# Kernel tuning notes

Hardware: AMD Instinct MI355X
Metric: run time of the kernel (lower is better)

Reference implementation:

```python
import jax, jax.numpy as jnp
import numpy as np

HID = 1024
PRED_LEN = 96


def lstm_cell(x, h, c, Wih, Whh, bih, bhh):
    # PyTorch LSTMCell: gates ordered i, f, g, o
    gates = x @ Wih.T + h @ Whh.T + bih + bhh
    i, f, g, o = jnp.split(gates, 4, axis=-1)
    c_new = jax.nn.sigmoid(f) * c + jax.nn.sigmoid(i) * jnp.tanh(g)
    h_new = jax.nn.sigmoid(o) * jnp.tanh(c_new)
    return h_new, c_new


def time_enc(idx, embs):
    # sum of 4 embedding lookups -> [..., time_encode_dim]
    return sum(e[idx[..., k]] for k, e in enumerate(embs))


def setup_inputs() -> dict:
    key = jax.random.key(0)
    ks = jax.random.split(key, 32)
    B, T, IN, OUT, H, TE = 256, 128, 7, 7, HID, 3
    d = {}
    d["x"] = jax.random.normal(ks[0], (B, T, IN), jnp.float32)
    d["y"] = jax.random.normal(ks[1], (B, PRED_LEN, OUT), jnp.float32)
    d["x_time_encode"] = jax.random.randint(ks[2], (B, T, 4), 0, 7)
    d["y_time_encode"] = jax.random.randint(ks[3], (B, PRED_LEN, 4), 0, 7)
    sizes = (12, 31, 24, 7)
    for i, n in enumerate(sizes):
        d[f"emb{i}"] = jax.random.normal(ks[4 + i], (n, TE), jnp.float32)
    ins = (IN + TE, H, H)
    s = float(1.0 / np.sqrt(H))
    for l in range(3):
        d[f"Wih{l}"] = jax.random.uniform(ks[8 + 4 * l], (4 * H, ins[l]), jnp.float32, -s, s)
        d[f"Whh{l}"] = jax.random.uniform(ks[9 + 4 * l], (4 * H, H), jnp.float32, -s, s)
        d[f"bih{l}"] = jax.random.uniform(ks[10 + 4 * l], (4 * H,), jnp.float32, -s, s)
        d[f"bhh{l}"] = jax.random.uniform(ks[11 + 4 * l], (4 * H,), jnp.float32, -s, s)
    d["fcW"] = jax.random.uniform(ks[20], (OUT, H), jnp.float32, -s, s)
    d["fcb"] = jax.random.uniform(ks[21], (OUT,), jnp.float32, -s, s)
    return d


def reference(x, y, x_time_encode, y_time_encode, emb0, emb1, emb2, emb3,
              Wih0, Whh0, bih0, bhh0, Wih1, Whh1, bih1, bhh1,
              Wih2, Whh2, bih2, bhh2, fcW, fcb):
    embs = (emb0, emb1, emb2, emb3)
    layers = ((Wih0, Whh0, bih0, bhh0),
              (Wih1, Whh1, bih1, bhh1),
              (Wih2, Whh2, bih2, bhh2))
    B = x.shape[0]
    H = Whh0.shape[1]

    # encode: concat time embedding, run stacked LSTM over time (dropout_rate=0 -> no-op)
    xin = jnp.concatenate([x, time_enc(x_time_encode, embs)], axis=-1)  # [B,T,in+te]
    h0 = tuple(jnp.zeros((B, H), x.dtype) for _ in range(3))

    def run_layers(hs, cs, inp):
        nh, nc = [], []
        for l, (Wih, Whh, bih, bhh) in enumerate(layers):
            h, c = lstm_cell(inp, hs[l], cs[l], Wih, Whh, bih, bhh)
            nh.append(h)
            nc.append(c)
            inp = h
        return tuple(nh), tuple(nc)

    def enc_step(carry, xt):
        hs, cs = carry
        hs, cs = run_layers(hs, cs, xt)
        return (hs, cs), None

    (hs, cs), _ = jax.lax.scan(enc_step, (h0, h0), xin.swapaxes(0, 1))

    y0 = hs[-1] @ fcW.T + fcb  # [B, out]

    def dec_step(carry, te_idx):
        hs, cs, y_prev = carry
        inp = jnp.concatenate([y_prev, time_enc(te_idx, embs)], axis=-1)
        hs, cs = run_layers(hs, cs, inp)
        yt = hs[-1] @ fcW.T + fcb
        return (hs, cs, yt), yt

    _, ys = jax.lax.scan(dec_step, (hs, cs, y0),
                         y_time_encode[:, :PRED_LEN - 1].swapaxes(0, 1))
    # [B, predict_len, out]
    return jnp.concatenate([y0[:, None], ys.swapaxes(0, 1)], axis=1)
```

## Files before the change

### kernel.cpp

```cpp
#include <hip/hip_runtime.h>

#define HID   1024
#define BATCH 256
#define TSEQ  128
#define PRED  96
#define IND   7
#define OUTD  7
#define SK    10

typedef __attribute__((ext_vector_type(8))) _Float16 f16x8;
typedef __attribute__((ext_vector_type(4))) float    f32x4;

#define BM   64
#define BN   64
#define GSTR 68

#define AUX_COH 17

__device__ __forceinline__ float sigmoidf_fast(float x) {
  return 1.0f / (1.0f + __expf(-x));
}
__device__ __forceinline__ float tanhf_fast(float x) {
  float ax = fabsf(x);
  float e  = __expf(-2.0f * ax);
  float r  = (1.0f - e) / (1.0f + e);
  return copysignf(r, x);
}

template<int AUX>
__device__ __forceinline__ void async_cp16(const void* g, void* l) {
  __builtin_amdgcn_global_load_lds(
      (const __attribute__((address_space(1))) void*)g,
      (__attribute__((address_space(3))) void*)l, 16, 0, AUX);
}

#define WBAR(N) asm volatile("s_waitcnt vmcnt(" #N ")\n\ts_barrier" ::: "memory")
#define BARO()  asm volatile("s_barrier" ::: "memory")

__device__ __forceinline__ void gridbar(unsigned* flags, unsigned* go,
                                        unsigned bc) {
  __syncthreads();
  const int tid = threadIdx.x;
  if (blockIdx.x == 0) {
    if (tid > 0) {
      while (__hip_atomic_load(flags + tid * 32,
                               __ATOMIC_RELAXED, __HIP_MEMORY_SCOPE_SYSTEM) < bc)
        __builtin_amdgcn_s_sleep(1);
    }
    __syncthreads();
    if (tid == 0)
      __hip_atomic_store(go, bc, __ATOMIC_RELAXED, __HIP_MEMORY_SCOPE_SYSTEM);
  } else {
    if (tid == 0) {
      __hip_atomic_store(flags + blockIdx.x * 32, bc,
                         __ATOMIC_RELAXED, __HIP_MEMORY_SCOPE_SYSTEM);
      while (__hip_atomic_load(go, __ATOMIC_RELAXED,
                               __HIP_MEMORY_SCOPE_SYSTEM) < bc)
        __builtin_amdgcn_s_sleep(1);
    }
    __syncthreads();
  }
}

__global__ __launch_bounds__(256) void prep_kernel(
    const float* __restrict__ Wih0, const float* __restrict__ Whh0,
    const float* __restrict__ bih0, const float* __restrict__ bhh0,
    const float* __restrict__ Wih1, const float* __restrict__ Whh1,
    const float* __restrict__ bih1, const float* __restrict__ bhh1,
    const float* __restrict__ Wih2, const float* __restrict__ Whh2,
    const float* __restrict__ bih2, const float* __restrict__ bhh2,
    _Float16* __restrict__ B0, _Float16* __restrict__ B1, _Float16* __restrict__ B2,
    float* __restrict__ W0p, float* __restrict__ biasP)
{
  size_t e = (size_t)blockIdx.x * 256 + threadIdx.x;
  const size_t S0 = (size_t)4096 * 1024;
  const size_t S1 = (size_t)4096 * 2048;
  if (e < S0) {
    int n = (int)(e >> 10), k = (int)(e & 1023);
    int nb = n >> 6, gate = (n >> 4) & 3, u = n & 15;
    int r = gate * 1024 + nb * 16 + u;
    B0[e] = (_Float16)Whh0[(size_t)r * 1024 + k];
  } else if (e < S0 + S1) {
    size_t q = e - S0;
    int n = (int)(q >> 11), k = (int)(q & 2047);
    int nb = n >> 6, gate = (n >> 4) & 3, u = n & 15;
    int r = gate * 1024 + nb * 16 + u;
    float v = (k < 1024) ? Wih1[(size_t)r * 1024 + k]
                         : Whh1[(size_t)r * 1024 + (k - 1024)];
    B1[q] = (_Float16)v;
  } else if (e < S0 + 2 * S1) {
    size_t q = e - S0 - S1;
    int n = (int)(q >> 11), k = (int)(q & 2047);
    int nb = n >> 6, gate = (n >> 4) & 3, u = n & 15;
    int r = gate * 1024 + nb * 16 + u;
    float v = (k < 1024) ? Wih2[(size_t)r * 1024 + k]
// ... 129 lines not shown

#pragma unroll
  for (int i = 0; i < 4; ++i) {
    int m = (tid >> 4) + i * 16;
    int u = tid & 15;
    float gi = Gs[m * GSTR + u];
    float gf = Gs[m * GSTR + 16 + u];
    float gg = Gs[m * GSTR + 32 + u];
    float go = Gs[m * GSTR + 48 + u];
    int nbase = nb * BN;
    gi += bias[nbase + u];
    gf += bias[nbase + 16 + u];
    gg += bias[nbase + 32 + u];
    go += bias[nbase + 48 + u];
    if (layer == 0) {
#pragma unroll
      for (int k = 0; k < SK; ++k) {
        float sv = SmallIn[m * SK + k];
        gi += sv * W0s[u * 11 + k];
        gf += sv * W0s[(16 + u) * 11 + k];
        gg += sv * W0s[(32 + u) * 11 + k];
        go += sv * W0s[(48 + u) * 11 + k];
      }
    }
    size_t cidx = (size_t)(Mbase + m) * HID + (size_t)nb * 16 + u;
    float cold = cst[cidx];
    float cn = sigmoidf_fast(gf) * cold + sigmoidf_fast(gi) * tanhf_fast(gg);
    float hn = sigmoidf_fast(go) * tanhf_fast(cn);
    cst[cidx] = cn;
    ho[cidx] = (_Float16)hn;
  }
}

template<int KC, int MODE>
__device__ __forceinline__ void dec_layer(
    const char* A1, const char* A2, const char* Bm,
    const int* a_off, const int* b_off, const int* l_off,
    char* smem, float* Gs, const float* SmallIn, const float* W0s,
    const float* biasg, float* creg, _Float16* hout, float* out,
    const float* w7, const float* fcadd, int s, int Mbase, int nb, int tid)
{
  const int w = tid >> 6, lane = tid & 63;
  const int quad = lane >> 4, l16 = lane & 15;
  f32x4 acc[4] = {};

#define DISSUE(c) do { \
    const char* Ab_ = (KC == 8 || (c) < 8) ? (A1 + (size_t)(c) * 256) \
                                           : (A2 + (size_t)((c) - 8) * 256); \
    const char* Bb_ = Bm + (size_t)(c) * 256; \
    char* Lb_ = smem + ((c) % 4) * 32768; \
    _Pragma("unroll") \
    for (int i_ = 0; i_ < 4; ++i_) { \
      async_cp16<AUX_COH>(Ab_ + a_off[i_], Lb_ + l_off[i_]); \
      async_cp16<0>(Bb_ + b_off[i_], Lb_ + 16384 + l_off[i_]); \
    } } while (0)

  DISSUE(0);
  DISSUE(1);
  DISSUE(2);
#pragma unroll
  for (int c = 0; c < KC; ++c) {
    if (c + 3 < KC)       { DISSUE(c + 3); WBAR(24); }
    else if (c + 3 == KC) { WBAR(16); }
    else if (c + 2 == KC) { WBAR(8); }
    else                  { WBAR(0); }
    const _Float16* As = (const _Float16*)(smem + (c % 4) * 32768);
    const _Float16* Bs = As + 8192;
#pragma unroll
    for (int ks = 0; ks < 4; ++ks) {
      int sq = (ks * 4 + quad) ^ l16;
      f16x8 bf = *reinterpret_cast<const f16x8*>(Bs + (w * 16 + l16) * 128 + sq * 8);
#pragma unroll
      for (int mt = 0; mt < 4; ++mt) {
        f16x8 af = *reinterpret_cast<const f16x8*>(As + (mt * 16 + l16) * 128 + sq * 8);
        acc[mt] = __builtin_amdgcn_mfma_f32_16x16x32_f16(af, bf, acc[mt], 0, 0, 0);
      }
    }
    BARO();
  }
#undef DISSUE

#pragma unroll
  for (int mt = 0; mt < 4; ++mt) {
    int row = mt * 16 + quad * 4;
    int col = w * 16 + l16;
#pragma unroll
    for (int r = 0; r < 4; ++r)
      Gs[(row + r) * GSTR + col] = acc[mt][r];
  }
  __syncthreads();

#pragma unroll
  for (int i = 0; i < 4; ++i) {
    int m = (tid >> 4) + i * 16;
    int u = tid & 15;
    float gi = Gs[m * GSTR + u]      + biasg[0];
    float gf = Gs[m * GSTR + 16 + u] + biasg[1];
    float gg = Gs[m * GSTR + 32 + u] + biasg[2];
    float go = Gs[m * GSTR + 48 + u] + biasg[3];
    if (MODE == 1) {
#pragma unroll
      for (int k = 0; k < SK; ++k) {
        float sv = SmallIn[m * SK + k];
        gi += sv * W0s[u * 11 + k];
        gf += sv * W0s[(16 + u) * 11 + k];
        gg += sv * W0s[(32 + u) * 11 + k];
        go += sv * W0s[(48 + u) * 11 + k];
      }
    }
    float cn = sigmoidf_fast(gf) * creg[i] + sigmoidf_fast(gi) * tanhf_fast(gg);
    float hn = sigmoidf_fast(go) * tanhf_fast(cn);
    creg[i] = cn;
    union { _Float16 f; unsigned short us; } cv; cv.f = (_Float16)hn;
    __hip_atomic_store(
        (unsigned short*)(hout + (size_t)(Mbase + m) * HID + (size_t)nb * 16 + u),
        cv.us, __ATOMIC_RELAXED, __HIP_MEMORY_SCOPE_SYSTEM);
    if (MODE == 3) {
#pragma unroll
      for (int o = 0; o < OUTD; ++o) {
        float r = hn * w7[o];
        r += __shfl_xor(r, 1, 16);
        r += __shfl_xor(r, 2, 16);
        r += __shfl_xor(r, 4, 16);
        r += __shfl_xor(r, 8, 16);
        if (u == 0)
          atomicAdd(&out[(size_t)(Mbase + m) * (PRED * OUTD) + (s + 1) * OUTD + o],
                    r + fcadd[o]);
      }
    }
  }
}

__global__ __launch_bounds__(256, 1) void lstm_dec(
    _Float16* __restrict__ h0a, _Float16* __restrict__ h0b,
    _Float16* __restrict__ h1a, _Float16* __restrict__ h1b,
    _Float16* __restrict__ h2a, _Float16* __restrict__ h2b,
    const _Float16* __restrict__ B0g, const _Float16* __restrict__ B1g,
    const _Float16* __restrict__ B2g,
    const float* __restrict__ biasP, const float* __restrict__ W0p,
    const float* __restrict__ cbuf,
    float* __restrict__ out, const int* __restrict__ yte,
    const float* __restrict__ e0, const float* __restrict__ e1,
    const float* __restrict__ e2, const float* __restrict__ e3,
    const float* __restrict__ fcW, const float* __restrict__ fcb,
    unsigned* __restrict__ flags, unsigned* __restrict__ go_w)
{
  __shared__ __align__(16) char smem[4 * 32768];
  __shared__ float Gs[BM * GSTR];
  __shared__ float SmallIn[BM * SK];
  __shared__ float W0s[BN * 11];

  const int tid = threadIdx.x;
  const int nb = blockIdx.x & 63, mb = blockIdx.x >> 6;
  const int Mbase = mb * BM;
  const int w = tid >> 6, lane = tid & 63;
  const int dr = lane >> 4, ds = lane & 15;

  int a_off[4], b1_off[4], b2_off[4], l_off[4];
#pragma unroll
  for (int i = 0; i < 4; ++i) {
    int lrow = w * 16 + i * 4 + dr;
    int sg = ds ^ (i * 4 + dr);
    a_off[i]  = (Mbase + lrow) * 2048 + sg * 16;
    b1_off[i] = (nb * 64 + lrow) * 2048 + sg * 16;
    b2_off[i] = (nb * 64 + lrow) * 4096 + sg * 16;
    l_off[i]  = lrow * 256 + ds * 16;
  }

  if (tid < BN) {
    const float* wp = W0p + (size_t)(nb * BN + tid) * SK;
#pragma unroll
    for (int i = 0; i < SK; ++i) W0s[tid * 11 + i] = wp[i];
  }

  const int u = tid & 15;
  float biasr[3][4];
#pragma unroll
  for (int l = 0; l < 3; ++l)
#pragma unroll
    for (int g = 0; g < 4; ++g)
      biasr[l][g] = biasP[l * 4096 + nb * 64 + g * 16 + u];

  float creg[3][4];
#pragma unroll
  for (int l = 0; l < 3; ++l)
#pragma unroll
    for (int i = 0; i < 4; ++i) {
      int m = (tid >> 4) + i * 16;
      creg[l][i] = cbuf[(size_t)l * 262144 + (size_t)(Mbase + m) * HID + nb * 16 + u];
    }

  float w7[OUTD], fcadd[OUTD];
#pragma unroll
  for (int o = 0; o < OUTD; ++o) {
    w7[o] = fcW[(size_t)o * HID + nb * 16 + u];
    fcadd[o] = (nb == 0) ? fcb[o] : 0.0f;
  }

  _Float16* h0[2] = {h0a, h0b};
  _Float16* h1[2] = {h1a, h1b};
  _Float16* h2[2] = {h2a, h2b};
  int p0 = 0, p1 = 1, p2 = 0;
  unsigned bc = 0;

  for (int s = 0; s < PRED - 1; ++s) {
    if (tid < BM) {
      int Mg = Mbase + tid;
      float v[SK];
      const float* yp = out + (size_t)Mg * (PRED * OUTD) + s * OUTD;
#pragma unroll
      for (int i = 0; i < OUTD; ++i)
        v[i] = __hip_atomic_load(yp + i, __ATOMIC_RELAXED,
                                 __HIP_MEMORY_SCOPE_SYSTEM);
      const int* ip = yte + ((size_t)Mg * PRED + s) * 4;
      int i0 = ip[0], i1 = ip[1], i2 = ip[2], i3 = ip[3];
#pragma unroll
      for (int dd = 0; dd < 3; ++dd)
        v[IND + dd] = e0[i0 * 3 + dd] + e1[i1 * 3 + dd] + e2[i2 * 3 + dd] + e3[i3 * 3 + dd];
#pragma unroll
      for (int i = 0; i < SK; ++i) SmallIn[tid * SK + i] = v[i];
    }

    dec_layer<8, 1>((const char*)h0[p0], (const char*)h0[p0], (const char*)B0g,
                    a_off, b1_off, l_off, smem, Gs, SmallIn, W0s,
                    biasr[0], creg[0], h0[1 - p0], out, w7, fcadd, s, Mbase, nb, tid);
    gridbar(flags, go_w, ++bc);

    dec_layer<16, 2>((const char*)h0[1 - p0], (const char*)h1[p1], (const char*)B1g,
                     a_off, b2_off, l_off, smem, Gs, SmallIn, W0s,
                     biasr[1], creg[1], h1[1 - p1], out, w7, fcadd, s, Mbase, nb, tid);
    gridbar(flags, go_w, ++bc);

    dec_layer<16, 3>((const char*)h1[1 - p1], (const char*)h2[p2], (const char*)B2g,
                     a_off, b2_off, l_off, smem, Gs, SmallIn, W0s,
                     biasr[2], creg[2], h2[1 - p2], out, w7, fcadd, s, Mbase, nb, tid);
    gridbar(flags, go_w, ++bc);

    p0 ^= 1; p1 ^= 1; p2 ^= 1;
  }
}

__global__ __launch_bounds__(256) void fc_kernel(
    const _Float16* __restrict__ h2, const float* __restrict__ fcW,
    const float* __restrict__ fcb, float* __restrict__ out)
{
  int wv = threadIdx.x >> 6, lane = threadIdx.x & 63;
  int row = blockIdx.x * 4 + wv;
  const _Float16* hp = h2 + (size_t)row * HID + lane * 16;
  float hv[16];
#pragma unroll
  for (int i = 0; i < 16; ++i) hv[i] = (float)hp[i];
  float acc[OUTD];
#pragma unroll
  for (int o = 0; o < OUTD; ++o) {
    const float* wp = fcW + (size_t)o * HID + lane * 16;
    float a = 0.f;
#pragma unroll
    for (int i = 0; i < 16; ++i) a += hv[i] * wp[i];
    acc[o] = a;
  }
#pragma unroll
  for (int o = 0; o < OUTD; ++o)
#pragma unroll
    for (int off = 32; off >= 1; off >>= 1)
      acc[o] += __shfl_xor(acc[o], off, 64);
  if (lane == 0) {
#pragma unroll
    for (int o = 0; o < OUTD; ++o)
      out[(size_t)row * (PRED * OUTD) + o] = acc[o] + fcb[o];
  }
}
// ... 3 lines not shown
                              hipStream_t stream) {
  const float* x   = (const float*)d_in[0];
  const int*   xte = (const int*)d_in[2];
  const int*   yte = (const int*)d_in[3];
  const float* e0  = (const float*)d_in[4];
  const float* e1  = (const float*)d_in[5];
  const float* e2  = (const float*)d_in[6];
  const float* e3  = (const float*)d_in[7];
  const float* Wih0 = (const float*)d_in[8];
  const float* Whh0 = (const float*)d_in[9];
  const float* bih0 = (const float*)d_in[10];
  const float* bhh0 = (const float*)d_in[11];
  const float* Wih1 = (const float*)d_in[12];
  const float* Whh1 = (const float*)d_in[13];
  const float* bih1 = (const float*)d_in[14];
  const float* bhh1 = (const float*)d_in[15];
  const float* Wih2 = (const float*)d_in[16];
  const float* Whh2 = (const float*)d_in[17];
  const float* bih2 = (const float*)d_in[18];
  const float* bhh2 = (const float*)d_in[19];
  const float* fcW = (const float*)d_in[20];
  const float* fcb = (const float*)d_in[21];
  float* out = (float*)d_out;

  char* ws = (char*)d_ws;
  _Float16* B0   = (_Float16*)(ws);
  _Float16* B1   = (_Float16*)(ws + 8388608);
  _Float16* B2   = (_Float16*)(ws + 25165824);
  float*    W0p  = (float*)(ws + 41943040);
  float*    biasP= (float*)(ws + 42106880);
  char*     hp0  = ws + 42156032;
  float*    cbuf = (float*)(ws + 43728896);
  char*     hp1  = ws + 46874624;
  unsigned* flags= (unsigned*)(ws + 48447488);
  unsigned* go_w = (unsigned*)(ws + 48480256);

  hipMemsetAsync(out, 0, (size_t)out_size * 4, stream);
  hipMemsetAsync(hp0, 0, 4718592, stream);
  hipMemsetAsync(hp1, 0, 1572864, stream);
  hipMemsetAsync(flags, 0, 32772, stream);

  prep_kernel<<<82128, 256, 0, stream>>>(Wih0, Whh0, bih0, bhh0,
                                         Wih1, Whh1, bih1, bhh1,
                                         Wih2, Whh2, bih2, bhh2,
                                         B0, B1, B2, W0p, biasP);

  auto hb = [&](int l, int par) -> _Float16* {
    return (_Float16*)((par ? hp1 : hp0) + (size_t)l * 524288);
  };
  float* cl[3] = {cbuf, cbuf + 262144, cbuf + 524288};

  for (int d = 0; d < TSEQ + 2; ++d) {
    lstm_wave<<<dim3(64, 12), 256, 0, stream>>>(
        d, hb(0,0), hb(0,1), hb(1,0), hb(1,1), hb(2,0), hb(2,1),
        B0, B1, B2, biasP, W0p, cl[0], cl[1], cl[2],
        x, xte, e0, e1, e2, e3);
  }

  fc_kernel<<<64, 256, 0, stream>>>(hb(2,0), fcW, fcb, out);

  lstm_dec<<<256, 256, 0, stream>>>(
      hb(0,0), hb(0,1), hb(1,0), hb(1,1), hb(2,0), hb(2,1),
      B0, B1, B2, biasP, W0p, cbuf,
      out, yte, e0, e1, e2, e3, fcW, fcb, flags, go_w);
}
```

Measured before the change: 8.073 ms.

## Split grid barrier into arrive/wait and overlap recurrent-half GEMM with barrier

The decode loop's grid barrier is split into a separate arrive and wait, and the centralized go-flag broadcast is dropped so each block polls all per-block flags directly. Each layer's recurrent-input half of the K loop (the chunks that read the block's own previous h, which is already complete) now runs before the barrier wait. The dependent half's first loads and the next layer's prefetch are issued before the epilogue. This is meant to hide grid-barrier latency and pipeline ramp-up behind useful MFMA work, at the cost of every block polling 255 flags and more complex cross-step buffer reuse that could hide a race.

```diff
diff --git a/kernel.cpp b/kernel.cpp
--- a/kernel.cpp
+++ b/kernel.cpp
@@ -36,30 +36,23 @@
 
 #define WBAR(N) asm volatile("s_waitcnt vmcnt(" #N ")\n\ts_barrier" ::: "memory")
 #define BARO()  asm volatile("s_barrier" ::: "memory")
-
-__device__ __forceinline__ void gridbar(unsigned* flags, unsigned* go,
-                                        unsigned bc) {
+#define LBAR()  asm volatile("s_waitcnt lgkmcnt(0)\n\ts_barrier" ::: "memory")
+
+__device__ __forceinline__ void bar_arrive(unsigned* flags, unsigned bc,
+                                           int tid, int bid) {
   __syncthreads();
-  const int tid = threadIdx.x;
-  if (blockIdx.x == 0) {
-    if (tid > 0) {
-      while (__hip_atomic_load(flags + tid * 32,
-                               __ATOMIC_RELAXED, __HIP_MEMORY_SCOPE_SYSTEM) < bc)
-        __builtin_amdgcn_s_sleep(1);
-    }
-    __syncthreads();
-    if (tid == 0)
-      __hip_atomic_store(go, bc, __ATOMIC_RELAXED, __HIP_MEMORY_SCOPE_SYSTEM);
-  } else {
-    if (tid == 0) {
-      __hip_atomic_store(flags + blockIdx.x * 32, bc,
-                         __ATOMIC_RELAXED, __HIP_MEMORY_SCOPE_SYSTEM);
-      while (__hip_atomic_load(go, __ATOMIC_RELAXED,
-                               __HIP_MEMORY_SCOPE_SYSTEM) < bc)
-        __builtin_amdgcn_s_sleep(1);
-    }
-    __syncthreads();
-  }
+  if (tid == 0)
+    __hip_atomic_store(flags + bid * 32, bc, __ATOMIC_RELAXED,
+                       __HIP_MEMORY_SCOPE_SYSTEM);
+}
+
+__device__ __forceinline__ void bar_wait(unsigned* flags, unsigned bc, int tid) {
+  if (bc) {
+    while (__hip_atomic_load(flags + tid * 32, __ATOMIC_RELAXED,
+                             __HIP_MEMORY_SCOPE_SYSTEM) < bc)
+      __builtin_amdgcn_s_sleep(1);
+  }
+  __syncthreads();
 }
 
 __global__ __launch_bounds__(256) void prep_kernel(
@@ -256,54 +249,63 @@
   }
 }
 
-template<int KC, int MODE>
-__device__ __forceinline__ void dec_layer(
+__device__ __forceinline__ void dissue(
+    int c, const char* A1, const char* A2, const char* Bm,
+    const int* a_off, const int* b_off, const int* l_off, char* smem)
+{
+  const char* Ab = (c < 8) ? (A1 + (size_t)c * 256)
+                           : (A2 + (size_t)(c - 8) * 256);
+  const char* Bb = Bm + (size_t)c * 256;
+  char* Lb = smem + (c & 3) * 32768;
+#pragma unroll
+  for (int i = 0; i < 4; ++i) {
+    async_cp16<AUX_COH>(Ab + a_off[i], Lb + l_off[i]);
+    async_cp16<0>(Bb + b_off[i], Lb + 16384 + l_off[i]);
+  }
+}
+
+__device__ __forceinline__ void consume(
+    int c, char* smem, f32x4 (&acc)[4], int w, int quad, int l16)
+{
+  const _Float16* As = (const _Float16*)(smem + (c & 3) * 32768);
+  const _Float16* Bs = As + 8192;
+#pragma unroll
+  for (int ks = 0; ks < 4; ++ks) {
+    int sq = (ks * 4 + quad) ^ l16;
+    f16x8 bf = *reinterpret_cast<const f16x8*>(Bs + (w * 16 + l16) * 128 + sq * 8);
+#pragma unroll
+    for (int mt = 0; mt < 4; ++mt) {
+      f16x8 af = *reinterpret_cast<const f16x8*>(As + (mt * 16 + l16) * 128 + sq * 8);
+      acc[mt] = __builtin_amdgcn_mfma_f32_16x16x32_f16(af, bf, acc[mt], 0, 0, 0);
+    }
+  }
+}
+
+template<int C0, int C1>
+__device__ __forceinline__ void seg_run(
     const char* A1, const char* A2, const char* Bm,
     const int* a_off, const int* b_off, const int* l_off,
-    char* smem, float* Gs, const float* SmallIn, const float* W0s,
+    char* smem, f32x4 (&acc)[4], int w, int quad, int l16)
+{
+#pragma unroll
+  for (int c = C0; c < C1; ++c) {
+    if (c + 3 < C1)       { dissue(c + 3, A1, A2, Bm, a_off, b_off, l_off, smem); WBAR(24); }
+    else if (c + 3 == C1) { WBAR(16); }
+    else if (c + 2 == C1) { WBAR(8); }
+    else                  { WBAR(0); }
+    consume(c, smem, acc, w, quad, l16);
+    BARO();
+  }
+}
+
+template<int MODE>
+__device__ __forceinline__ void epilogue(
+    f32x4 (&acc)[4], float* Gs, const float* SmallIn, const float* W0s,
     const float* biasg, float* creg, _Float16* hout, float* out,
     const float* w7, const float* fcadd, int s, int Mbase, int nb, int tid)
 {
   const int w = tid >> 6, lane = tid & 63;
   const int quad = lane >> 4, l16 = lane & 15;
-  f32x4 acc[4] = {};
-
-#define DISSUE(c) do { \
-    const char* Ab_ = (KC == 8 || (c) < 8) ? (A1 + (size_t)(c) * 256) \
-                                           : (A2 + (size_t)((c) - 8) * 256); \
-    const char* Bb_ = Bm + (size_t)(c) * 256; \
-    char* Lb_ = smem + ((c) % 4) * 32768; \
-    _Pragma("unroll") \
-    for (int i_ = 0; i_ < 4; ++i_) { \
-      async_cp16<AUX_COH>(Ab_ + a_off[i_], Lb_ + l_off[i_]); \
-      async_cp16<0>(Bb_ + b_off[i_], Lb_ + 16384 + l_off[i_]); \
-    } } while (0)
-
-  DISSUE(0);
-  DISSUE(1);
-  DISSUE(2);
-#pragma unroll
-  for (int c = 0; c < KC; ++c) {
-    if (c + 3 < KC)       { DISSUE(c + 3); WBAR(24); }
-    else if (c + 3 == KC) { WBAR(16); }
-    else if (c + 2 == KC) { WBAR(8); }
-    else                  { WBAR(0); }
-    const _Float16* As = (const _Float16*)(smem + (c % 4) * 32768);
-    const _Float16* Bs = As + 8192;
-#pragma unroll
-    for (int ks = 0; ks < 4; ++ks) {
-      int sq = (ks * 4 + quad) ^ l16;
-      f16x8 bf = *reinterpret_cast<const f16x8*>(Bs + (w * 16 + l16) * 128 + sq * 8);
-#pragma unroll
-      for (int mt = 0; mt < 4; ++mt) {
-        f16x8 af = *reinterpret_cast<const f16x8*>(As + (mt * 16 + l16) * 128 + sq * 8);
-        acc[mt] = __builtin_amdgcn_mfma_f32_16x16x32_f16(af, bf, acc[mt], 0, 0, 0);
-      }
-    }
-    BARO();
-  }
-#undef DISSUE
-
 #pragma unroll
   for (int mt = 0; mt < 4; ++mt) {
     int row = mt * 16 + quad * 4;
@@ -312,8 +314,7 @@
     for (int r = 0; r < 4; ++r)
       Gs[(row + r) * GSTR + col] = acc[mt][r];
   }
-  __syncthreads();
-
+  LBAR();
 #pragma unroll
   for (int i = 0; i < 4; ++i) {
     int m = (tid >> 4) + i * 16;
@@ -374,10 +375,13 @@
   __shared__ float SmallIn[BM * SK];
   __shared__ float W0s[BN * 11];
 
+  (void)go_w;
   const int tid = threadIdx.x;
-  const int nb = blockIdx.x & 63, mb = blockIdx.x >> 6;
+  const int bid = blockIdx.x;
+  const int nb = bid & 63, mb = bid >> 6;
   const int Mbase = mb * BM;
   const int w = tid >> 6, lane = tid & 63;
+  const int quad = lane >> 4, l16 = lane & 15;
   const int dr = lane >> 4, ds = lane & 15;
 
   int a_off[4], b1_off[4], b2_off[4], l_off[4];
@@ -427,38 +431,89 @@
   int p0 = 0, p1 = 1, p2 = 0;
   unsigned bc = 0;
 
+  const char* cB0 = (const char*)B0g;
+  const char* cB1 = (const char*)B1g;
+  const char* cB2 = (const char*)B2g;
+
+  {
+    const char* A = (const char*)h0[p0];
+    dissue(0, A, A, cB0, a_off, b1_off, l_off, smem);
+    dissue(1, A, A, cB0, a_off, b1_off, l_off, smem);
+    dissue(2, A, A, cB0, a_off, b1_off, l_off, smem);
+  }
+
+#pragma unroll 1
   for (int s = 0; s < PRED - 1; ++s) {
-    if (tid < BM) {
-      int Mg = Mbase + tid;
+    const char* hA0  = (const char*)h0[p0];
+    const char* hA0n = (const char*)h0[1 - p0];
+    const char* hA1  = (const char*)h1[p1];
+    const char* hA1n = (const char*)h1[1 - p1];
+    const char* hA2  = (const char*)h2[p2];
+
+    {
+      f32x4 acc[4] = {};
+      seg_run<0, 8>(hA0, hA0, cB0, a_off, b1_off, l_off, smem, acc, w, quad, l16);
+      bar_wait(flags, bc, tid);
       float v[SK];
-      const float* yp = out + (size_t)Mg * (PRED * OUTD) + s * OUTD;
-#pragma unroll
-      for (int i = 0; i < OUTD; ++i)
-        v[i] = __hip_atomic_load(yp + i, __ATOMIC_RELAXED,
-                                 __HIP_MEMORY_SCOPE_SYSTEM);
-      const int* ip = yte + ((size_t)Mg * PRED + s) * 4;
-      int i0 = ip[0], i1 = ip[1], i2 = ip[2], i3 = ip[3];
-#pragma unroll
-      for (int dd = 0; dd < 3; ++dd)
-        v[IND + dd] = e0[i0 * 3 + dd] + e1[i1 * 3 + dd] + e2[i2 * 3 + dd] + e3[i3 * 3 + dd];
-#pragma unroll
-      for (int i = 0; i < SK; ++i) SmallIn[tid * SK + i] = v[i];
-    }
-
-    dec_layer<8, 1>((const char*)h0[p0], (const char*)h0[p0], (const char*)B0g,
-                    a_off, b1_off, l_off, smem, Gs, SmallIn, W0s,
-                    biasr[0], creg[0], h0[1 - p0], out, w7, fcadd, s, Mbase, nb, tid);
-    gridbar(flags, go_w, ++bc);
-
-    dec_layer<16, 2>((const char*)h0[1 - p0], (const char*)h1[p1], (const char*)B1g,
-                     a_off, b2_off, l_off, smem, Gs, SmallIn, W0s,
-                     biasr[1], creg[1], h1[1 - p1], out, w7, fcadd, s, Mbase, nb, tid);
-    gridbar(flags, go_w, ++bc);
-
-    dec_layer<16, 3>((const char*)h1[1 - p1], (const char*)h2[p2], (const char*)B2g,
-                     a_off, b2_off, l_off, smem, Gs, SmallIn, W0s,
-                     biasr[2], creg[2], h2[1 - p2], out, w7, fcadd, s, Mbase, nb, tid);
-    gridbar(flags, go_w, ++bc);
+      if (tid < BM) {
+        const float* yp = out + (size_t)(Mbase + tid) * (PRED * OUTD) + s * OUTD;
+#pragma unroll
+        for (int i = 0; i < OUTD; ++i)
+          v[i] = __hip_atomic_load(yp + i, __ATOMIC_RELAXED,
+                                   __HIP_MEMORY_SCOPE_SYSTEM);
+        const int* ip = yte + ((size_t)(Mbase + tid) * PRED + s) * 4;
+        int i0 = ip[0], i1 = ip[1], i2 = ip[2], i3 = ip[3];
+#pragma unroll
+        for (int dd = 0; dd < 3; ++dd)
+          v[IND + dd] = e0[i0 * 3 + dd] + e1[i1 * 3 + dd]
+                      + e2[i2 * 3 + dd] + e3[i3 * 3 + dd];
+      }
+      dissue(8,  hA0n, hA1, cB1, a_off, b2_off, l_off, smem);
+      dissue(9,  hA0n, hA1, cB1, a_off, b2_off, l_off, smem);
+      dissue(10, hA0n, hA1, cB1, a_off, b2_off, l_off, smem);
+      if (tid < BM) {
+#pragma unroll
+        for (int i = 0; i < SK; ++i) SmallIn[tid * SK + i] = v[i];
+      }
+      epilogue<1>(acc, Gs, SmallIn, W0s, biasr[0], creg[0], h0[1 - p0], out,
+                  w7, fcadd, s, Mbase, nb, tid);
+      bar_arrive(flags, ++bc, tid, bid);
+    }
+
+    {
+      f32x4 acc[4] = {};
+      seg_run<8, 16>(hA0n, hA1, cB1, a_off, b2_off, l_off, smem, acc, w, quad, l16);
+      bar_wait(flags, bc, tid);
+      dissue(0, hA0n, hA1, cB1, a_off, b2_off, l_off, smem);
+      dissue(1, hA0n, hA1, cB1, a_off, b2_off, l_off, smem);
+      dissue(2, hA0n, hA1, cB1, a_off, b2_off, l_off, smem);
+      seg_run<0, 8>(hA0n, hA1, cB1, a_off, b2_off, l_off, smem, acc, w, quad, l16);
+      dissue(8,  hA1n, hA2, cB2, a_off, b2_off, l_off, smem);
+      dissue(9,  hA1n, hA2, cB2, a_off, b2_off, l_off, smem);
+      dissue(10, hA1n, hA2, cB2, a_off, b2_off, l_off, smem);
+      epilogue<2>(acc, Gs, SmallIn, W0s, biasr[1], creg[1], h1[1 - p1], out,
+                  w7, fcadd, s, Mbase, nb, tid);
+      bar_arrive(flags, ++bc, tid, bid);
+    }
+
+    {
+      f32x4 acc[4] = {};
+      seg_run<8, 16>(hA1n, hA2, cB2, a_off, b2_off, l_off, smem, acc, w, quad, l16);
+      bar_wait(flags, bc, tid);
+      dissue(0, hA1n, hA2, cB2, a_off, b2_off, l_off, smem);
+      dissue(1, hA1n, hA2, cB2, a_off, b2_off, l_off, smem);
+      dissue(2, hA1n, hA2, cB2, a_off, b2_off, l_off, smem);
+      seg_run<0, 8>(hA1n, hA2, cB2, a_off, b2_off, l_off, smem, acc, w, quad, l16);
+      if (s + 1 < PRED - 1) {
+        const char* An = (const char*)h0[p0 ^ 1];
+        dissue(0, An, An, cB0, a_off, b1_off, l_off, smem);
+        dissue(1, An, An, cB0, a_off, b1_off, l_off, smem);
+        dissue(2, An, An, cB0, a_off, b1_off, l_off, smem);
+      }
+      epilogue<3>(acc, Gs, SmallIn, W0s, biasr[2], creg[2], h2[1 - p2], out,
+                  w7, fcadd, s, Mbase, nb, tid);
+      bar_arrive(flags, ++bc, tid, bid);
+    }
 
     p0 ^= 1; p1 ^= 1; p2 ^= 1;
   }
```

Result: no change. 8.113 ms (+0.5%).

## Retile decoder LSTM GEMM to 32x128 blocks with 3-stage async pipeline

Applied to the files above, without the earlier changes.

The persistent decoder kernel now gives each block a 32-row by 128-column tile instead of 64x64, and shrinks the LDS ring from four to three stages. Each wave computes a 2x2 set of MFMA tiles, so every A and B fragment load feeds two MFMAs. The gate epilogue, cell-state mapping, bias and FC reduction indices are remapped so each block owns two 64-column gate groups. The trade-off: h-state reads per block drop, but each weight slice is now read by twice as many blocks, which doubles the weight traffic through L2.

```diff
diff --git a/kernel.cpp b/kernel.cpp
--- a/kernel.cpp
+++ b/kernel.cpp
@@ -14,6 +14,11 @@
 #define BM   64
 #define BN   64
 #define GSTR 68
+
+#define DBM  32
+#define DBN  128
+#define DSTR 132
+#define DSLOT 40960
 
 #define AUX_COH 17
 
@@ -259,77 +264,81 @@
 template<int KC, int MODE>
 __device__ __forceinline__ void dec_layer(
     const char* A1, const char* A2, const char* Bm,
-    const int* a_off, const int* b_off, const int* l_off,
+    const int* a_off, const int* b_off,
     char* smem, float* Gs, const float* SmallIn, const float* W0s,
     const float* biasg, float* creg, _Float16* hout, float* out,
     const float* w7, const float* fcadd, int s, int Mbase, int nb, int tid)
 {
   const int w = tid >> 6, lane = tid & 63;
   const int quad = lane >> 4, l16 = lane & 15;
-  f32x4 acc[4] = {};
+  f32x4 acc[2][2] = {};
 
 #define DISSUE(c) do { \
     const char* Ab_ = (KC == 8 || (c) < 8) ? (A1 + (size_t)(c) * 256) \
                                            : (A2 + (size_t)((c) - 8) * 256); \
     const char* Bb_ = Bm + (size_t)(c) * 256; \
-    char* Lb_ = smem + ((c) % 4) * 32768; \
+    char* Lb_ = smem + ((c) % 3) * DSLOT; \
     _Pragma("unroll") \
-    for (int i_ = 0; i_ < 4; ++i_) { \
-      async_cp16<AUX_COH>(Ab_ + a_off[i_], Lb_ + l_off[i_]); \
-      async_cp16<0>(Bb_ + b_off[i_], Lb_ + 16384 + l_off[i_]); \
-    } } while (0)
+    for (int i_ = 0; i_ < 2; ++i_) \
+      async_cp16<AUX_COH>(Ab_ + a_off[i_], Lb_ + i_ * 4096 + tid * 16); \
+    _Pragma("unroll") \
+    for (int i_ = 0; i_ < 8; ++i_) \
+      async_cp16<0>(Bb_ + b_off[i_], Lb_ + 8192 + i_ * 4096 + tid * 16); \
+  } while (0)
 
   DISSUE(0);
   DISSUE(1);
-  DISSUE(2);
 #pragma unroll
   for (int c = 0; c < KC; ++c) {
-    if (c + 3 < KC)       { DISSUE(c + 3); WBAR(24); }
-    else if (c + 3 == KC) { WBAR(16); }
-    else if (c + 2 == KC) { WBAR(8); }
+    if (c + 2 < KC)       { DISSUE(c + 2); WBAR(20); }
+    else if (c + 2 == KC) { WBAR(10); }
     else                  { WBAR(0); }
-    const _Float16* As = (const _Float16*)(smem + (c % 4) * 32768);
-    const _Float16* Bs = As + 8192;
+    const _Float16* As = (const _Float16*)(smem + (c % 3) * DSLOT);
+    const _Float16* Bs = As + 4096;
 #pragma unroll
     for (int ks = 0; ks < 4; ++ks) {
       int sq = (ks * 4 + quad) ^ l16;
-      f16x8 bf = *reinterpret_cast<const f16x8*>(Bs + (w * 16 + l16) * 128 + sq * 8);
-#pragma unroll
-      for (int mt = 0; mt < 4; ++mt) {
-        f16x8 af = *reinterpret_cast<const f16x8*>(As + (mt * 16 + l16) * 128 + sq * 8);
-        acc[mt] = __builtin_amdgcn_mfma_f32_16x16x32_f16(af, bf, acc[mt], 0, 0, 0);
-      }
+      f16x8 a0 = *reinterpret_cast<const f16x8*>(As + l16 * 128 + sq * 8);
+      f16x8 a1 = *reinterpret_cast<const f16x8*>(As + (16 + l16) * 128 + sq * 8);
+      f16x8 b0 = *reinterpret_cast<const f16x8*>(Bs + (w * 32 + l16) * 128 + sq * 8);
+      f16x8 b1 = *reinterpret_cast<const f16x8*>(Bs + (w * 32 + 16 + l16) * 128 + sq * 8);
+      acc[0][0] = __builtin_amdgcn_mfma_f32_16x16x32_f16(a0, b0, acc[0][0], 0, 0, 0);
+      acc[0][1] = __builtin_amdgcn_mfma_f32_16x16x32_f16(a0, b1, acc[0][1], 0, 0, 0);
+      acc[1][0] = __builtin_amdgcn_mfma_f32_16x16x32_f16(a1, b0, acc[1][0], 0, 0, 0);
+      acc[1][1] = __builtin_amdgcn_mfma_f32_16x16x32_f16(a1, b1, acc[1][1], 0, 0, 0);
     }
     BARO();
   }
 #undef DISSUE
 
 #pragma unroll
-  for (int mt = 0; mt < 4; ++mt) {
-    int row = mt * 16 + quad * 4;
-    int col = w * 16 + l16;
-#pragma unroll
-    for (int r = 0; r < 4; ++r)
-      Gs[(row + r) * GSTR + col] = acc[mt][r];
-  }
+  for (int mt = 0; mt < 2; ++mt)
+#pragma unroll
+    for (int nt = 0; nt < 2; ++nt) {
+      int col = w * 32 + nt * 16 + l16;
+#pragma unroll
+      for (int r = 0; r < 4; ++r)
+        Gs[(mt * 16 + quad * 4 + r) * DSTR + col] = acc[mt][nt][r];
+    }
   __syncthreads();
 
+  const int u = tid & 15, g = (tid >> 4) & 1, mr = tid >> 5;
 #pragma unroll
   for (int i = 0; i < 4; ++i) {
-    int m = (tid >> 4) + i * 16;
-    int u = tid & 15;
-    float gi = Gs[m * GSTR + u]      + biasg[0];
-    float gf = Gs[m * GSTR + 16 + u] + biasg[1];
-    float gg = Gs[m * GSTR + 32 + u] + biasg[2];
-    float go = Gs[m * GSTR + 48 + u] + biasg[3];
+    int m = mr + i * 8;
+    const float* gp = Gs + m * DSTR + g * 64;
+    float gi = gp[u]      + biasg[0];
+    float gf = gp[16 + u] + biasg[1];
+    float gg = gp[32 + u] + biasg[2];
+    float go = gp[48 + u] + biasg[3];
     if (MODE == 1) {
 #pragma unroll
       for (int k = 0; k < SK; ++k) {
         float sv = SmallIn[m * SK + k];
-        gi += sv * W0s[u * 11 + k];
-        gf += sv * W0s[(16 + u) * 11 + k];
-        gg += sv * W0s[(32 + u) * 11 + k];
-        go += sv * W0s[(48 + u) * 11 + k];
+        gi += sv * W0s[(g * 64 + u) * 11 + k];
+        gf += sv * W0s[(g * 64 + 16 + u) * 11 + k];
+        gg += sv * W0s[(g * 64 + 32 + u) * 11 + k];
+        go += sv * W0s[(g * 64 + 48 + u) * 11 + k];
       }
     }
     float cn = sigmoidf_fast(gf) * creg[i] + sigmoidf_fast(gi) * tanhf_fast(gg);
@@ -337,17 +346,18 @@
     creg[i] = cn;
     union { _Float16 f; unsigned short us; } cv; cv.f = (_Float16)hn;
     __hip_atomic_store(
-        (unsigned short*)(hout + (size_t)(Mbase + m) * HID + (size_t)nb * 16 + u),
+        (unsigned short*)(hout + (size_t)(Mbase + m) * HID + nb * 32 + g * 16 + u),
         cv.us, __ATOMIC_RELAXED, __HIP_MEMORY_SCOPE_SYSTEM);
     if (MODE == 3) {
 #pragma unroll
       for (int o = 0; o < OUTD; ++o) {
         float r = hn * w7[o];
-        r += __shfl_xor(r, 1, 16);
-        r += __shfl_xor(r, 2, 16);
-        r += __shfl_xor(r, 4, 16);
-        r += __shfl_xor(r, 8, 16);
-        if (u == 0)
+        r += __shfl_xor(r, 1, 32);
+        r += __shfl_xor(r, 2, 32);
+        r += __shfl_xor(r, 4, 32);
+        r += __shfl_xor(r, 8, 32);
+        r += __shfl_xor(r, 16, 32);
+        if ((tid & 31) == 0)
           atomicAdd(&out[(size_t)(Mbase + m) * (PRED * OUTD) + (s + 1) * OUTD + o],
                     r + fcadd[o]);
       }
@@ -369,56 +379,62 @@
     const float* __restrict__ fcW, const float* __restrict__ fcb,
     unsigned* __restrict__ flags, unsigned* __restrict__ go_w)
 {
-  __shared__ __align__(16) char smem[4 * 32768];
-  __shared__ float Gs[BM * GSTR];
-  __shared__ float SmallIn[BM * SK];
-  __shared__ float W0s[BN * 11];
+  __shared__ __align__(16) char smem[3 * DSLOT];
+  __shared__ float Gs[DBM * DSTR];
+  __shared__ float SmallIn[DBM * SK];
+  __shared__ float W0s[DBN * 11];
 
   const int tid = threadIdx.x;
-  const int nb = blockIdx.x & 63, mb = blockIdx.x >> 6;
-  const int Mbase = mb * BM;
-  const int w = tid >> 6, lane = tid & 63;
-  const int dr = lane >> 4, ds = lane & 15;
-
-  int a_off[4], b1_off[4], b2_off[4], l_off[4];
-#pragma unroll
-  for (int i = 0; i < 4; ++i) {
-    int lrow = w * 16 + i * 4 + dr;
-    int sg = ds ^ (i * 4 + dr);
-    a_off[i]  = (Mbase + lrow) * 2048 + sg * 16;
-    b1_off[i] = (nb * 64 + lrow) * 2048 + sg * 16;
-    b2_off[i] = (nb * 64 + lrow) * 4096 + sg * 16;
-    l_off[i]  = lrow * 256 + ds * 16;
-  }
-
-  if (tid < BN) {
-    const float* wp = W0p + (size_t)(nb * BN + tid) * SK;
+  const int bid = blockIdx.x;
+  const int nb = bid & 31, mb = bid >> 5;
+  const int Mbase = mb * DBM;
+
+  int a_off[2];
+#pragma unroll
+  for (int op = 0; op < 2; ++op) {
+    int j = op * 256 + tid;
+    int row = j >> 4, ds = j & 15;
+    a_off[op] = (Mbase + row) * 2048 + ((ds ^ (row & 15)) * 16);
+  }
+  int b1_off[8], b2_off[8];
+#pragma unroll
+  for (int op = 0; op < 8; ++op) {
+    int j = op * 256 + tid;
+    int row = j >> 4, ds = j & 15;
+    int sw = (ds ^ (row & 15)) * 16;
+    b1_off[op] = (nb * DBN + row) * 2048 + sw;
+    b2_off[op] = (nb * DBN + row) * 4096 + sw;
+  }
+
+  if (tid < DBN) {
+    const float* wp = W0p + (size_t)(nb * DBN + tid) * SK;
 #pragma unroll
     for (int i = 0; i < SK; ++i) W0s[tid * 11 + i] = wp[i];
   }
 
-  const int u = tid & 15;
+  const int u = tid & 15, g = (tid >> 4) & 1, mr = tid >> 5;
   float biasr[3][4];
 #pragma unroll
   for (int l = 0; l < 3; ++l)
 #pragma unroll
-    for (int g = 0; g < 4; ++g)
-      biasr[l][g] = biasP[l * 4096 + nb * 64 + g * 16 + u];
+    for (int gate = 0; gate < 4; ++gate)
+      biasr[l][gate] = biasP[l * 4096 + nb * DBN + g * 64 + gate * 16 + u];
 
   float creg[3][4];
 #pragma unroll
   for (int l = 0; l < 3; ++l)
 #pragma unroll
     for (int i = 0; i < 4; ++i) {
-      int m = (tid >> 4) + i * 16;
-      creg[l][i] = cbuf[(size_t)l * 262144 + (size_t)(Mbase + m) * HID + nb * 16 + u];
+      int m = mr + i * 8;
+      creg[l][i] = cbuf[(size_t)l * 262144 + (size_t)(Mbase + m) * HID
+                        + nb * 32 + g * 16 + u];
     }
 
   float w7[OUTD], fcadd[OUTD];
 #pragma unroll
   for (int o = 0; o < OUTD; ++o) {
-    w7[o] = fcW[(size_t)o * HID + nb * 16 + u];
-    fcadd[o] = (nb == 0) ? fcb[o] : 0.0f;
+    w7[o] = fcW[(size_t)o * HID + nb * 32 + g * 16 + u];
+    fcadd[o] = (nb == 0 && g == 0) ? fcb[o] : 0.0f;
   }
 
   _Float16* h0[2] = {h0a, h0b};
@@ -428,7 +444,7 @@
   unsigned bc = 0;
 
   for (int s = 0; s < PRED - 1; ++s) {
-    if (tid < BM) {
+    if (tid < DBM) {
       int Mg = Mbase + tid;
       float v[SK];
       const float* yp = out + (size_t)Mg * (PRED * OUTD) + s * OUTD;
@@ -446,17 +462,17 @@
     }
 
     dec_layer<8, 1>((const char*)h0[p0], (const char*)h0[p0], (const char*)B0g,
-                    a_off, b1_off, l_off, smem, Gs, SmallIn, W0s,
+                    a_off, b1_off, smem, Gs, SmallIn, W0s,
                     biasr[0], creg[0], h0[1 - p0], out, w7, fcadd, s, Mbase, nb, tid);
     gridbar(flags, go_w, ++bc);
 
     dec_layer<16, 2>((const char*)h0[1 - p0], (const char*)h1[p1], (const char*)B1g,
-                     a_off, b2_off, l_off, smem, Gs, SmallIn, W0s,
+                     a_off, b2_off, smem, Gs, SmallIn, W0s,
                      biasr[1], creg[1], h1[1 - p1], out, w7, fcadd, s, Mbase, nb, tid);
     gridbar(flags, go_w, ++bc);
 
     dec_layer<16, 3>((const char*)h1[1 - p1], (const char*)h2[p2], (const char*)B2g,
-                     a_off, b2_off, l_off, smem, Gs, SmallIn, W0s,
+                     a_off, b2_off, smem, Gs, SmallIn, W0s,
                      biasr[2], creg[2], h2[1 - p2], out, w7, fcadd, s, Mbase, nb, tid);
     gridbar(flags, go_w, ++bc);
 
```

Result: slower. 11.88 ms (+47.1%).

## Replace persistent decoder with grid barriers by per-layer kernel launches

Applied to the files above, without the earlier changes.

The persistent decoder kernel, which used a software grid barrier between layers, is replaced by one kernel launch per layer per decode step (285 launches). Each launch uses a 64x8 grid with 32-row M tiles, double buffering instead of a 4-stage pipeline, and two blocks per CU. Cell state moves from registers to global memory, and bias and FC weights are reloaded on every launch. This removes the spin-wait barrier latency but adds launch overhead, a shallower pipeline and extra global traffic per step.

```diff
diff --git a/kernel.cpp b/kernel.cpp
--- a/kernel.cpp
+++ b/kernel.cpp
@@ -15,8 +15,6 @@
 #define BN   64
 #define GSTR 68
 
-#define AUX_COH 17
-
 __device__ __forceinline__ float sigmoidf_fast(float x) {
   return 1.0f / (1.0f + __expf(-x));
 }
@@ -36,31 +34,6 @@
 
 #define WBAR(N) asm volatile("s_waitcnt vmcnt(" #N ")\n\ts_barrier" ::: "memory")
 #define BARO()  asm volatile("s_barrier" ::: "memory")
-
-__device__ __forceinline__ void gridbar(unsigned* flags, unsigned* go,
-                                        unsigned bc) {
-  __syncthreads();
-  const int tid = threadIdx.x;
-  if (blockIdx.x == 0) {
-    if (tid > 0) {
-      while (__hip_atomic_load(flags + tid * 32,
-                               __ATOMIC_RELAXED, __HIP_MEMORY_SCOPE_SYSTEM) < bc)
-        __builtin_amdgcn_s_sleep(1);
-    }
-    __syncthreads();
-    if (tid == 0)
-      __hip_atomic_store(go, bc, __ATOMIC_RELAXED, __HIP_MEMORY_SCOPE_SYSTEM);
-  } else {
-    if (tid == 0) {
-      __hip_atomic_store(flags + blockIdx.x * 32, bc,
-                         __ATOMIC_RELAXED, __HIP_MEMORY_SCOPE_SYSTEM);
-      while (__hip_atomic_load(go, __ATOMIC_RELAXED,
-                               __HIP_MEMORY_SCOPE_SYSTEM) < bc)
-        __builtin_amdgcn_s_sleep(1);
-    }
-    __syncthreads();
-  }
-}
 
 __global__ __launch_bounds__(256) void prep_kernel(
     const float* __restrict__ Wih0, const float* __restrict__ Whh0,
@@ -257,55 +230,101 @@
 }
 
 template<int KC, int MODE>
-__device__ __forceinline__ void dec_layer(
-    const char* A1, const char* A2, const char* Bm,
-    const int* a_off, const int* b_off, const int* l_off,
-    char* smem, float* Gs, const float* SmallIn, const float* W0s,
-    const float* biasg, float* creg, _Float16* hout, float* out,
-    const float* w7, const float* fcadd, int s, int Mbase, int nb, int tid)
+__global__ __launch_bounds__(256, 2) void dec_phase(
+    const _Float16* __restrict__ A1g, const _Float16* __restrict__ A2g,
+    _Float16* __restrict__ ho, const _Float16* __restrict__ Bm,
+    const float* __restrict__ biasL, const float* __restrict__ W0p,
+    float* __restrict__ cst, float* __restrict__ out,
+    const int* __restrict__ yte,
+    const float* __restrict__ e0, const float* __restrict__ e1,
+    const float* __restrict__ e2, const float* __restrict__ e3,
+    const float* __restrict__ fcW, const float* __restrict__ fcb, int s)
 {
+  __shared__ __align__(16) char smem[2 * 24576];
+  __shared__ float Gs[32 * GSTR];
+  __shared__ float SmallIn[32 * SK];
+  __shared__ float W0s[64 * 11];
+
+  const int tid = threadIdx.x;
+  const int nb = blockIdx.x, mb = blockIdx.y;
+  const int Mbase = mb * 32;
+
+  if (MODE == 1) {
+    if (tid < 32) {
+      int Mg = Mbase + tid;
+      float v[SK];
+      const float* yp = out + (size_t)Mg * (PRED * OUTD) + s * OUTD;
+#pragma unroll
+      for (int i = 0; i < OUTD; ++i) v[i] = yp[i];
+      const int* ip = yte + ((size_t)Mg * PRED + s) * 4;
+      int i0 = ip[0], i1 = ip[1], i2 = ip[2], i3 = ip[3];
+#pragma unroll
+      for (int dd = 0; dd < 3; ++dd)
+        v[IND + dd] = e0[i0 * 3 + dd] + e1[i1 * 3 + dd]
+                    + e2[i2 * 3 + dd] + e3[i3 * 3 + dd];
+#pragma unroll
+      for (int i = 0; i < SK; ++i) SmallIn[tid * SK + i] = v[i];
+    }
+    if (tid < 64) {
+      const float* wp = W0p + (size_t)(nb * 64 + tid) * SK;
+#pragma unroll
+      for (int i = 0; i < SK; ++i) W0s[tid * 11 + i] = wp[i];
+    }
+  }
+
   const int w = tid >> 6, lane = tid & 63;
   const int quad = lane >> 4, l16 = lane & 15;
-  f32x4 acc[4] = {};
-
-#define DISSUE(c) do { \
-    const char* Ab_ = (KC == 8 || (c) < 8) ? (A1 + (size_t)(c) * 256) \
-                                           : (A2 + (size_t)((c) - 8) * 256); \
-    const char* Bb_ = Bm + (size_t)(c) * 256; \
-    char* Lb_ = smem + ((c) % 4) * 32768; \
+
+  int a_src[2], a_dst[2], b_src[4], b_dst[4];
+#pragma unroll
+  for (int op = 0; op < 2; ++op) {
+    int j = op * 256 + tid, row = j >> 4, seg = j & 15;
+    a_src[op] = (Mbase + row) * 2048 + ((seg ^ (row & 15)) * 16);
+    a_dst[op] = row * 256 + seg * 16;
+  }
+#pragma unroll
+  for (int op = 0; op < 4; ++op) {
+    int j = op * 256 + tid, row = j >> 4, seg = j & 15;
+    b_src[op] = (nb * 64 + row) * (KC * 256) + ((seg ^ (row & 15)) * 16);
+    b_dst[op] = 8192 + row * 256 + seg * 16;
+  }
+
+#define PISSUE(c) do { \
+    const char* Ab_ = (KC == 8 || (c) < 8) \
+        ? ((const char*)A1g + (size_t)(c) * 256) \
+        : ((const char*)A2g + (size_t)((c) - 8) * 256); \
+    const char* Bb_ = (const char*)Bm + (size_t)(c) * 256; \
+    char* L_ = smem + ((c) & 1) * 24576; \
     _Pragma("unroll") \
-    for (int i_ = 0; i_ < 4; ++i_) { \
-      async_cp16<AUX_COH>(Ab_ + a_off[i_], Lb_ + l_off[i_]); \
-      async_cp16<0>(Bb_ + b_off[i_], Lb_ + 16384 + l_off[i_]); \
-    } } while (0)
-
-  DISSUE(0);
-  DISSUE(1);
-  DISSUE(2);
+    for (int i_ = 0; i_ < 2; ++i_) async_cp16<0>(Ab_ + a_src[i_], L_ + a_dst[i_]); \
+    _Pragma("unroll") \
+    for (int i_ = 0; i_ < 4; ++i_) async_cp16<0>(Bb_ + b_src[i_], L_ + b_dst[i_]); \
+  } while (0)
+
+  f32x4 acc[2] = {};
+  PISSUE(0);
 #pragma unroll
   for (int c = 0; c < KC; ++c) {
-    if (c + 3 < KC)       { DISSUE(c + 3); WBAR(24); }
-    else if (c + 3 == KC) { WBAR(16); }
-    else if (c + 2 == KC) { WBAR(8); }
-    else                  { WBAR(0); }
-    const _Float16* As = (const _Float16*)(smem + (c % 4) * 32768);
-    const _Float16* Bs = As + 8192;
+    if (c + 1 < KC) { PISSUE(c + 1); WBAR(6); }
+    else            { WBAR(0); }
+    const _Float16* As = (const _Float16*)(smem + (c & 1) * 24576);
+    const _Float16* Bs = As + 4096;
 #pragma unroll
     for (int ks = 0; ks < 4; ++ks) {
       int sq = (ks * 4 + quad) ^ l16;
       f16x8 bf = *reinterpret_cast<const f16x8*>(Bs + (w * 16 + l16) * 128 + sq * 8);
 #pragma unroll
-      for (int mt = 0; mt < 4; ++mt) {
+      for (int mt = 0; mt < 2; ++mt) {
         f16x8 af = *reinterpret_cast<const f16x8*>(As + (mt * 16 + l16) * 128 + sq * 8);
         acc[mt] = __builtin_amdgcn_mfma_f32_16x16x32_f16(af, bf, acc[mt], 0, 0, 0);
       }
     }
     BARO();
   }
-#undef DISSUE
-
-#pragma unroll
-  for (int mt = 0; mt < 4; ++mt) {
+#undef PISSUE
+
+#pragma unroll
+  for (int mt = 0; mt < 2; ++mt) {
     int row = mt * 16 + quad * 4;
     int col = w * 16 + l16;
 #pragma unroll
@@ -314,14 +333,15 @@
   }
   __syncthreads();
 
-#pragma unroll
-  for (int i = 0; i < 4; ++i) {
+  const int u = tid & 15;
+#pragma unroll
+  for (int i = 0; i < 2; ++i) {
     int m = (tid >> 4) + i * 16;
-    int u = tid & 15;
-    float gi = Gs[m * GSTR + u]      + biasg[0];
-    float gf = Gs[m * GSTR + 16 + u] + biasg[1];
-    float gg = Gs[m * GSTR + 32 + u] + biasg[2];
-    float go = Gs[m * GSTR + 48 + u] + biasg[3];
+    int nbase = nb * 64;
+    float gi = Gs[m * GSTR + u]      + biasL[nbase + u];
+    float gf = Gs[m * GSTR + 16 + u] + biasL[nbase + 16 + u];
+    float gg = Gs[m * GSTR + 32 + u] + biasL[nbase + 32 + u];
+    float go = Gs[m * GSTR + 48 + u] + biasL[nbase + 48 + u];
     if (MODE == 1) {
 #pragma unroll
       for (int k = 0; k < SK; ++k) {
@@ -332,135 +352,25 @@
         go += sv * W0s[(48 + u) * 11 + k];
       }
     }
-    float cn = sigmoidf_fast(gf) * creg[i] + sigmoidf_fast(gi) * tanhf_fast(gg);
+    size_t cidx = (size_t)(Mbase + m) * HID + (size_t)nb * 16 + u;
+    float cold = cst[cidx];
+    float cn = sigmoidf_fast(gf) * cold + sigmoidf_fast(gi) * tanhf_fast(gg);
     float hn = sigmoidf_fast(go) * tanhf_fast(cn);
-    creg[i] = cn;
-    union { _Float16 f; unsigned short us; } cv; cv.f = (_Float16)hn;
-    __hip_atomic_store(
-        (unsigned short*)(hout + (size_t)(Mbase + m) * HID + (size_t)nb * 16 + u),
-        cv.us, __ATOMIC_RELAXED, __HIP_MEMORY_SCOPE_SYSTEM);
+    cst[cidx] = cn;
+    ho[cidx] = (_Float16)hn;
     if (MODE == 3) {
 #pragma unroll
       for (int o = 0; o < OUTD; ++o) {
-        float r = hn * w7[o];
+        float r = hn * fcW[(size_t)o * HID + nb * 16 + u];
         r += __shfl_xor(r, 1, 16);
         r += __shfl_xor(r, 2, 16);
         r += __shfl_xor(r, 4, 16);
         r += __shfl_xor(r, 8, 16);
         if (u == 0)
           atomicAdd(&out[(size_t)(Mbase + m) * (PRED * OUTD) + (s + 1) * OUTD + o],
-                    r + fcadd[o]);
+                    r + ((nb == 0) ? fcb[o] : 0.0f));
       }
     }
-  }
-}
-
-__global__ __launch_bounds__(256, 1) void lstm_dec(
-    _Float16* __restrict__ h0a, _Float16* __restrict__ h0b,
-    _Float16* __restrict__ h1a, _Float16* __restrict__ h1b,
-    _Float16* __restrict__ h2a, _Float16* __restrict__ h2b,
-    const _Float16* __restrict__ B0g, const _Float16* __restrict__ B1g,
-    const _Float16* __restrict__ B2g,
-    const float* __restrict__ biasP, const float* __restrict__ W0p,
-    const float* __restrict__ cbuf,
-    float* __restrict__ out, const int* __restrict__ yte,
-    const float* __restrict__ e0, const float* __restrict__ e1,
-    const float* __restrict__ e2, const float* __restrict__ e3,
-    const float* __restrict__ fcW, const float* __restrict__ fcb,
-    unsigned* __restrict__ flags, unsigned* __restrict__ go_w)
-{
-  __shared__ __align__(16) char smem[4 * 32768];
-  __shared__ float Gs[BM * GSTR];
-  __shared__ float SmallIn[BM * SK];
-  __shared__ float W0s[BN * 11];
-
-  const int tid = threadIdx.x;
-  const int nb = blockIdx.x & 63, mb = blockIdx.x >> 6;
-  const int Mbase = mb * BM;
-  const int w = tid >> 6, lane = tid & 63;
-  const int dr = lane >> 4, ds = lane & 15;
-
-  int a_off[4], b1_off[4], b2_off[4], l_off[4];
-#pragma unroll
-  for (int i = 0; i < 4; ++i) {
-    int lrow = w * 16 + i * 4 + dr;
-    int sg = ds ^ (i * 4 + dr);
-    a_off[i]  = (Mbase + lrow) * 2048 + sg * 16;
-    b1_off[i] = (nb * 64 + lrow) * 2048 + sg * 16;
-    b2_off[i] = (nb * 64 + lrow) * 4096 + sg * 16;
-    l_off[i]  = lrow * 256 + ds * 16;
-  }
-
-  if (tid < BN) {
-    const float* wp = W0p + (size_t)(nb * BN + tid) * SK;
-#pragma unroll
-    for (int i = 0; i < SK; ++i) W0s[tid * 11 + i] = wp[i];
-  }
-
-  const int u = tid & 15;
-  float biasr[3][4];
-#pragma unroll
-  for (int l = 0; l < 3; ++l)
-#pragma unroll
-    for (int g = 0; g < 4; ++g)
-      biasr[l][g] = biasP[l * 4096 + nb * 64 + g * 16 + u];
-
-  float creg[3][4];
-#pragma unroll
-  for (int l = 0; l < 3; ++l)
-#pragma unroll
-    for (int i = 0; i < 4; ++i) {
-      int m = (tid >> 4) + i * 16;
-      creg[l][i] = cbuf[(size_t)l * 262144 + (size_t)(Mbase + m) * HID + nb * 16 + u];
-    }
-
-  float w7[OUTD], fcadd[OUTD];
-#pragma unroll
-  for (int o = 0; o < OUTD; ++o) {
-    w7[o] = fcW[(size_t)o * HID + nb * 16 + u];
-    fcadd[o] = (nb == 0) ? fcb[o] : 0.0f;
-  }
-
-  _Float16* h0[2] = {h0a, h0b};
-  _Float16* h1[2] = {h1a, h1b};
-  _Float16* h2[2] = {h2a, h2b};
-  int p0 = 0, p1 = 1, p2 = 0;
-  unsigned bc = 0;
-
-  for (int s = 0; s < PRED - 1; ++s) {
-    if (tid < BM) {
-      int Mg = Mbase + tid;
-      float v[SK];
-      const float* yp = out + (size_t)Mg * (PRED * OUTD) + s * OUTD;
-#pragma unroll
-      for (int i = 0; i < OUTD; ++i)
-        v[i] = __hip_atomic_load(yp + i, __ATOMIC_RELAXED,
-                                 __HIP_MEMORY_SCOPE_SYSTEM);
-      const int* ip = yte + ((size_t)Mg * PRED + s) * 4;
-      int i0 = ip[0], i1 = ip[1], i2 = ip[2], i3 = ip[3];
-#pragma unroll
-      for (int dd = 0; dd < 3; ++dd)
-        v[IND + dd] = e0[i0 * 3 + dd] + e1[i1 * 3 + dd] + e2[i2 * 3 + dd] + e3[i3 * 3 + dd];
-#pragma unroll
-      for (int i = 0; i < SK; ++i) SmallIn[tid * SK + i] = v[i];
-    }
-
-    dec_layer<8, 1>((const char*)h0[p0], (const char*)h0[p0], (const char*)B0g,
-                    a_off, b1_off, l_off, smem, Gs, SmallIn, W0s,
-                    biasr[0], creg[0], h0[1 - p0], out, w7, fcadd, s, Mbase, nb, tid);
-    gridbar(flags, go_w, ++bc);
-
-    dec_layer<16, 2>((const char*)h0[1 - p0], (const char*)h1[p1], (const char*)B1g,
-                     a_off, b2_off, l_off, smem, Gs, SmallIn, W0s,
-                     biasr[1], creg[1], h1[1 - p1], out, w7, fcadd, s, Mbase, nb, tid);
-    gridbar(flags, go_w, ++bc);
-
-    dec_layer<16, 3>((const char*)h1[1 - p1], (const char*)h2[p2], (const char*)B2g,
-                     a_off, b2_off, l_off, smem, Gs, SmallIn, W0s,
-                     biasr[2], creg[2], h2[1 - p2], out, w7, fcadd, s, Mbase, nb, tid);
-    gridbar(flags, go_w, ++bc);
-
-    p0 ^= 1; p1 ^= 1; p2 ^= 1;
   }
 }
 
@@ -530,13 +440,10 @@
   char*     hp0  = ws + 42156032;
   float*    cbuf = (float*)(ws + 43728896);
   char*     hp1  = ws + 46874624;
-  unsigned* flags= (unsigned*)(ws + 48447488);
-  unsigned* go_w = (unsigned*)(ws + 48480256);
 
   hipMemsetAsync(out, 0, (size_t)out_size * 4, stream);
   hipMemsetAsync(hp0, 0, 4718592, stream);
   hipMemsetAsync(hp1, 0, 1572864, stream);
-  hipMemsetAsync(flags, 0, 32772, stream);
 
   prep_kernel<<<82128, 256, 0, stream>>>(Wih0, Whh0, bih0, bhh0,
                                          Wih1, Whh1, bih1, bhh1,
@@ -557,8 +464,18 @@
 
   fc_kernel<<<64, 256, 0, stream>>>(hb(2,0), fcW, fcb, out);
 
-  lstm_dec<<<256, 256, 0, stream>>>(
-      hb(0,0), hb(0,1), hb(1,0), hb(1,1), hb(2,0), hb(2,1),
-      B0, B1, B2, biasP, W0p, cbuf,
-      out, yte, e0, e1, e2, e3, fcW, fcb, flags, go_w);
-}
+  int p0 = 0, p1 = 1, p2 = 0;
+  const dim3 dgrid(64, 8);
+  for (int s = 0; s < PRED - 1; ++s) {
+    dec_phase<8, 1><<<dgrid, 256, 0, stream>>>(
+        hb(0, p0), hb(0, p0), hb(0, 1 - p0), B0,
+        biasP, W0p, cl[0], out, yte, e0, e1, e2, e3, fcW, fcb, s);
+    dec_phase<16, 2><<<dgrid, 256, 0, stream>>>(
+        hb(0, 1 - p0), hb(1, p1), hb(1, 1 - p1), B1,
+        biasP + 4096, W0p, cl[1], out, yte, e0, e1, e2, e3, fcW, fcb, s);
+    dec_phase<16, 3><<<dgrid, 256, 0, stream>>>(
+        hb(1, 1 - p1), hb(2, p2), hb(2, 1 - p2), B2,
+        biasP + 8192, W0p, cl[2], out, yte, e0, e1, e2, e3, fcW, fcb, s);
+    p0 ^= 1; p1 ^= 1; p2 ^= 1;
+  }
+}
```

Measured after the change: 7.808 ms. -3.3%, faster.
